# Kernel tuning notes

Hardware: AMD Instinct MI355X
Metric: run time of the kernel (lower is better)

The kernel has to match this reference:

```python
import jax, jax.numpy as jnp
import numpy as np

BN_EPS = 1e-5
POOL_EPS = 1e-6


def conv3x3(x, w, b):
    # x: (N,C,H,W), w: (O,C,3,3) -> (N,O,H,W), stride 1, SAME padding
    y = jax.lax.conv_general_dilated(x, w, window_strides=(1, 1), padding='SAME',
                                     dimension_numbers=('NCHW', 'OIHW', 'NCHW'))
    return y + b[None, :, None, None]


def deform_conv2d(x, off_w, off_b, mod_w, mod_b, w, b):
    # Modulated deformable conv (DCNv2), 3x3, stride 1, padding 1 (torchvision semantics).
    N, C, H, W = x.shape
    off = conv3x3(x, off_w, off_b).reshape(N, 9, 2, H, W)  # per-tap (dy, dx)
    mod = 2.0 * jax.nn.sigmoid(conv3x3(x, mod_w, mod_b))   # (N,9,H,W)
    dy = (jnp.arange(3, dtype=x.dtype) - 1.0).repeat(3)    # tap k = ky*3+kx
    dx = jnp.tile(jnp.arange(3, dtype=x.dtype) - 1.0, 3)
    py = off[:, :, 0] + dy[None, :, None, None] + jnp.arange(H, dtype=x.dtype)[None, None, :, None]
    px = off[:, :, 1] + dx[None, :, None, None] + jnp.arange(W, dtype=x.dtype)[None, None, None, :]
    y0f = jnp.floor(py); x0f = jnp.floor(px)
    wy = py - y0f; wx = px - x0f
    y0 = y0f.astype(jnp.int32); x0 = x0f.astype(jnp.int32)
    flat = x.reshape(N, C, H * W)

    def gather(yi, xi):
        # zero padding outside the image
        valid = ((yi >= 0) & (yi < H) & (xi >= 0) & (xi < W)).astype(x.dtype)
        idx = jnp.clip(yi, 0, H - 1) * W + jnp.clip(xi, 0, W - 1)      # (N,9,H,W)
        idx_b = jnp.broadcast_to(idx.reshape(N, 1, -1), (N, C, 9 * H * W))
        g = jnp.take_along_axis(flat, idx_b, axis=2).reshape(N, C, 9, H, W)
        return g * valid[:, None]

    s = (gather(y0, x0) * ((1 - wy) * (1 - wx))[:, None]
         + gather(y0, x0 + 1) * ((1 - wy) * wx)[:, None]
         + gather(y0 + 1, x0) * (wy * (1 - wx))[:, None]
         + gather(y0 + 1, x0 + 1) * (wy * wx)[:, None])       # (N,C,9,H,W)
    out = jnp.einsum('nckij,nkij,ock->noij', s, mod, w.reshape(w.shape[0], C, 9))
    return out + b[None, :, None, None]


def setup_inputs() -> dict:
    key = jax.random.key(0)
    ks = jax.random.split(key, 20)
    b, n_f, n_i, Hm, Wm = 2, 8, 10, 192, 192
    C_in, C_dcn, n_inc, n_pix = 256, 64, 128, 64
    h, w = 96, 96
    f32 = jnp.float32
    inp = {
        'x': jax.random.normal(ks[0], (b * n_f, C_in, h, w), f32),
        'masks': jax.random.uniform(ks[1], (b, n_f, n_i, Hm, Wm), f32),
        'conv1_w': jax.random.normal(ks[2], (C_dcn, C_in, 3, 3), f32) * 0.02,
        'conv1_b': jnp.zeros((C_dcn,), f32),
        'bn_gamma': jnp.ones((C_dcn,), f32),
        'bn_beta': jnp.zeros((C_dcn,), f32),
        'bn_mean': jax.random.normal(ks[3], (C_dcn,), f32) * 0.01,
        'bn_var': jnp.ones((C_dcn,), f32),
        'off_w': jax.random.normal(ks[4], (18, C_dcn, 3, 3), f32) * 0.01,
        'off_b': jnp.zeros((18,), f32),
        'mod_w': jax.random.normal(ks[5], (9, C_dcn, 3, 3), f32) * 0.01,
        'mod_b': jnp.zeros((9,), f32),
        'dcn_w': jax.random.normal(ks[6], (C_dcn, C_dcn, 3, 3), f32) * 0.05,
        'dcn_b': jnp.zeros((C_dcn,), f32),
        'smooth_w': jax.random.normal(ks[7], (C_dcn, C_dcn), f32) * 0.05,
        'smooth_b': jnp.zeros((C_dcn,), f32),
        'inc_w': jax.random.normal(ks[8], (n_inc, C_dcn), f32) * 0.05,
        'pix_w': jax.random.normal(ks[9], (n_pix, C_dcn), f32) * 0.05,
    }
    return inp


def reference(x, masks, conv1_w, conv1_b, bn_gamma, bn_beta, bn_mean, bn_var,
              off_w, off_b, mod_w, mod_b, dcn_w, dcn_b,
              smooth_w, smooth_b, inc_w, pix_w):
    # conv1: Conv3x3 + BatchNorm (eval stats) + ReLU
    y = conv3x3(x, conv1_w, conv1_b)
    y = (y - bn_mean[None, :, None, None]) * (bn_gamma[None, :, None, None]
        * jax.lax.rsqrt(bn_var + BN_EPS)[None, :, None, None]) + bn_beta[None, :, None, None]
    y = jax.nn.relu(y)
    # deformable conv
    y = deform_conv2d(y, off_w, off_b, mod_w, mod_b, dcn_w, dcn_b)

    b, n_f, n_i, Hm, Wm = masks.shape
    N, C, h, w = y.shape
    # resizeAnyShape -> bilinear, align_corners=False
    m = jax.image.resize(masks.reshape(b * n_f * n_i, Hm, Wm),
                         (b * n_f * n_i, h, w), method='bilinear', antialias=False)
    m = m.reshape(b, n_f, n_i, h * w)
    xf = y.reshape(b, n_f, C, h * w)
    # mask-weighted spatial average: avoid (b,n_f,n_i,C,h*w) intermediate
    num = jnp.einsum('bfcp,bfip->bfic', xf, m)            # (b,n_f,n_i,C)
    den = m.sum(axis=-1)[..., None]                        # (b,n_f,n_i,1)
    feat = num / (den + POOL_EPS)
    feat = jax.nn.relu(feat @ smooth_w.T + smooth_b)
    inc_kernels = feat @ inc_w.T
    pix_kernels = feat @ pix_w.T
    return (inc_kernels, pix_kernels)
```

## Files before the change

kernel.cpp:

```cpp
#include <hip/hip_runtime.h>
#include <hip/hip_bf16.h>

typedef __attribute__((ext_vector_type(8))) __bf16 bf16x8;
typedef __attribute__((ext_vector_type(4))) float f32x4;
typedef __attribute__((ext_vector_type(4))) unsigned int u32x4;
typedef __attribute__((ext_vector_type(4))) unsigned short u16x4;
typedef __attribute__((ext_vector_type(8))) unsigned short ushort8;
typedef __attribute__((ext_vector_type(4))) int i32x4;

#define MFMA16(a,b,c) __builtin_amdgcn_mfma_f32_16x16x32_bf16((a),(b),(c),0,0,0)

__device__ __forceinline__ float b2f(unsigned short u) {
  union { unsigned int i; float f; } v; v.i = ((unsigned int)u) << 16; return v.f;
}
__device__ __forceinline__ unsigned short f2b(float f) {
  union { float f; unsigned int u; } v; v.f = f;
  unsigned int u = v.u;
  unsigned int r = (u + 0x7fffu + ((u >> 16) & 1u)) >> 16;
  return (unsigned short)r;
}

#define NIMG 16
#define CIN  256
#define CD   64
#define HH   96
#define WW   96
#define HW   (HH*WW)

#define OFF_Y1   (0ll)
#define OFF_Y2   (18874368ll)
#define OFF_OFF  (37748736ll)
#define OFF_MOD  (48365568ll)
#define OFF_M    (53673984ll)
#define OFF_NP   OFF_OFF
#define OFF_DP   (OFF_OFF + 1310720ll)
#define OFF_SBN  (59908096ll)
#define OFF_TBN  (59908352ll)
#define OFF_W1   (59908608ll)
#define OFF_W2   (60203520ll)
#define OFF_W3   (60240384ll)
#define WS_NEEDED (60314112ll)

__global__ void k_prep(const float* __restrict__ conv1_w, const float* __restrict__ conv1_b,
                       const float* __restrict__ bn_gamma, const float* __restrict__ bn_beta,
                       const float* __restrict__ bn_mean, const float* __restrict__ bn_var,
                       const float* __restrict__ off_w, const float* __restrict__ mod_w,
                       const float* __restrict__ dcn_w,
                       unsigned short* __restrict__ w1, unsigned short* __restrict__ w2,
                       unsigned short* __restrict__ w3,
                       float* __restrict__ sbn, float* __restrict__ tbn)
{
  int e = blockIdx.x * 256 + threadIdx.x;
  if (e < 147456) {
    int j = e & 7, o = (e >> 3) & 63, cg = (e >> 9) & 31, t = e >> 14;
    w1[e] = f2b(conv1_w[(o * 256 + cg * 8 + j) * 9 + t]);
  } else if (e < 147456 + 18432) {
    int i = e - 147456;
    int j = i & 7, o = (i >> 3) & 31, cg = (i >> 8) & 7, t = i >> 11;
    int ch = cg * 8 + j;
    float v = 0.f;
    if (o < 18)      v = off_w[(o * 64 + ch) * 9 + t];
    else if (o < 27) v = mod_w[((o - 18) * 64 + ch) * 9 + t];
    w2[i] = f2b(v);
  } else if (e < 147456 + 18432 + 36864) {
    int i = e - 147456 - 18432;
    int j = i & 7, o = (i >> 3) & 63, cg = (i >> 9) & 7, t = i >> 12;
    w3[i] = f2b(dcn_w[(o * 64 + cg * 8 + j) * 9 + t]);
  } else {
    int i = e - (147456 + 18432 + 36864);
    if (i < 64) {
      sbn[i] = bn_gamma[i] * rsqrtf(bn_var[i] + 1e-5f);
    } else if (i < 128) {
      int q = i - 64;
      float s = bn_gamma[q] * rsqrtf(bn_var[q] + 1e-5f);
      tbn[q] = (conv1_b[q] - bn_mean[q]) * s + bn_beta[q];
    }
  }
}

__global__ __launch_bounds__(256)
void k_conv1(const float* __restrict__ x, const unsigned short* __restrict__ w1,
             const float* __restrict__ sbn, const float* __restrict__ tbn,
             unsigned short* __restrict__ y1)
{
  __shared__ __align__(16) unsigned short xs[4][98][48];
  __shared__ __align__(16) unsigned short As[9 * 4 * 64 * 8];

  const int tid = threadIdx.x;
  const int lane = tid & 63, wv = tid >> 6;
  const int l16 = lane & 15, lg = lane >> 4;
  const int wrow = wv & 1, wch = wv >> 1;
  const int h0 = blockIdx.x * 2;
  const int n = blockIdx.y;
  const float* xn = x + (size_t)n * CIN * HW;

  f32x4 acc[2][6];
  #pragma unroll
  for (int a = 0; a < 2; ++a)
    #pragma unroll
    for (int b = 0; b < 6; ++b) { f32x4 z = {0.f,0.f,0.f,0.f}; acc[a][b] = z; }

  for (int chunk = 0; chunk < 8; ++chunk) {
    const int c0 = chunk * 32;
    __syncthreads();
    #pragma unroll
    for (int it = 0; it < 12; ++it) {
      int idx = tid + it * 256;
      int c = idx & 31;
      int w4 = (idx >> 5) % 24;
      int r = idx / 768;
      int row = h0 - 1 + r;
      f32x4 v = {0.f,0.f,0.f,0.f};
      if (row >= 0 && row < HH)
        v = *reinterpret_cast<const f32x4*>(xn + (c0 + c) * HW + row * WW + w4 * 4);
      int wp = w4 * 4 + 1;
      xs[r][wp + 0][c] = f2b(v[0]);
      xs[r][wp + 1][c] = f2b(v[1]);
      xs[r][wp + 2][c] = f2b(v[2]);
      xs[r][wp + 3][c] = f2b(v[3]);
      if (w4 == 0)  xs[r][0][c]  = 0;
      if (w4 == 23) xs[r][97][c] = 0;
    }
    #pragma unroll
    for (int it = 0; it < 9; ++it) {
      int idx = tid + it * 256;
      int o = idx & 63, g = (idx >> 6) & 3, t = idx >> 8;
      *reinterpret_cast<u32x4*>(&As[((t * 4 + g) * 64 + o) * 8]) =
        *reinterpret_cast<const u32x4*>(&w1[((t * 32 + chunk * 4 + g) * 64 + o) * 8]);
    }
    __syncthreads();
    #pragma unroll
    for (int t = 0; t < 9; ++t) {
      const int ky = t / 3, kx = t % 3;
      bf16x8 a0 = *reinterpret_cast<const bf16x8*>(&As[((t*4 + lg)*64 + wch*32 + l16)*8]);
      bf16x8 a1 = *reinterpret_cast<const bf16x8*>(&As[((t*4 + lg)*64 + wch*32 + 16 + l16)*8]);
      const int r = wrow + ky;
      #pragma unroll
      for (int wt = 0; wt < 6; ++wt) {
        bf16x8 b = *reinterpret_cast<const bf16x8*>(&xs[r][wt*16 + l16 + kx][lg*8]);
        acc[0][wt] = MFMA16(a0, b, acc[0][wt]);
        acc[1][wt] = MFMA16(a1, b, acc[1][wt]);
      }
    }
  }
  __syncthreads();
  unsigned short* ys = &xs[0][0][0];
  #pragma unroll
  for (int ct = 0; ct < 2; ++ct) {
    #pragma unroll
    for (int j = 0; j < 4; ++j) {
      int o = wch * 32 + ct * 16 + lg * 4 + j;
      float s = sbn[o], tt = tbn[o];
      #pragma unroll
      for (int wt = 0; wt < 6; ++wt) {
        float v = acc[ct][wt][j] * s + tt;
        v = v > 0.f ? v : 0.f;
        ys[((wrow * 96 + wt * 16 + l16) * 72) + o] = f2b(v);
      }
    }
  }
  __syncthreads();
  #pragma unroll
  for (int it = 0; it < 6; ++it) {
    int idx = tid + it * 256;
    int cg = idx & 7, p = (idx >> 3) % 96, r = idx / 768;
    *reinterpret_cast<u32x4*>(&y1[(((size_t)(n * HH + h0 + r)) * WW + p) * 64 + cg * 8]) =
      *reinterpret_cast<const u32x4*>(&ys[(r * 96 + p) * 72 + cg * 8]);
  }
}

__global__ __launch_bounds__(256)
void k_conv2(const unsigned short* __restrict__ y1, const unsigned short* __restrict__ w2,
             const float* __restrict__ off_b, const float* __restrict__ mod_b,
             float* __restrict__ off_o, float* __restrict__ mod_o)
{
  __shared__ __align__(16) unsigned short xs[4][98][48];

  const int tid = threadIdx.x;
  const int lane = tid & 63, wv = tid >> 6;
  const int l16 = lane & 15, lg = lane >> 4;
  const int wrow = wv & 1, wct = wv >> 1;
  const int h0 = blockIdx.x * 2;
  const int n = blockIdx.y;
  const unsigned short* y1n = y1 + (size_t)n * HW * CD;

  bf16x8 aR[2][9];
  #pragma unroll
  for (int ch = 0; ch < 2; ++ch)
    #pragma unroll
    for (int t = 0; t < 9; ++t)
      aR[ch][t] = *reinterpret_cast<const bf16x8*>(
          &w2[((t * 8 + ch * 4 + lg) * 32 + wct * 16 + l16) * 8]);

  f32x4 acc[6];
  #pragma unroll
  for (int b = 0; b < 6; ++b) { f32x4 z = {0.f,0.f,0.f,0.f}; acc[b] = z; }

  #pragma unroll
  for (int chunk = 0; chunk < 2; ++chunk) {
    const int c0 = chunk * 32;
    __syncthreads();
    #pragma unroll
    for (int it = 0; it < 6; ++it) {
      int idx = tid + it * 256;
      int cg = idx & 3, w = (idx >> 2) % 96, r = idx / 384;
      int row = h0 - 1 + r;
      u32x4 v = {0u,0u,0u,0u};
      if (row >= 0 && row < HH)
        v = *reinterpret_cast<const u32x4*>(&y1n[((size_t)row * WW + w) * 64 + c0 + cg * 8]);
      *reinterpret_cast<u32x4*>(&xs[r][w + 1][cg * 8]) = v;
    }
    if (tid < 32) {
      int r = tid >> 3, side = (tid >> 2) & 1, cg = tid & 3;
      u32x4 z = {0u,0u,0u,0u};
      *reinterpret_cast<u32x4*>(&xs[r][side * 97][cg * 8]) = z;
    }
    __syncthreads();
    #pragma unroll
    for (int t = 0; t < 9; ++t) {
      const int ky = t / 3, kx = t % 3;
      const int r = wrow + ky;
      #pragma unroll
      for (int wt = 0; wt < 6; ++wt) {
        bf16x8 b = *reinterpret_cast<const bf16x8*>(&xs[r][wt*16 + l16 + kx][lg*8]);
        acc[wt] = MFMA16(aR[chunk][t], b, acc[wt]);
      }
    }
  }
  const int h = h0 + wrow;
  #pragma unroll
  for (int j = 0; j < 4; ++j) {
    int o = wct * 16 + lg * 4 + j;
    if (o < 18) {
      float bo = off_b[o];
      #pragma unroll
      for (int wt = 0; wt < 6; ++wt)
        off_o[((n * 18 + o) * HH + h) * WW + wt * 16 + l16] = acc[wt][j] + bo;
    } else if (o < 27) {
      int q = o - 18;
      float bo = mod_b[q];
      #pragma unroll
      for (int wt = 0; wt < 6; ++wt) {
        float v = acc[wt][j] + bo;
        mod_o[((n * 9 + q) * HH + h) * WW + wt * 16 + l16] = 2.f / (1.f + expf(-v));
      }
    }
  }
}

__global__ __launch_bounds__(256)
void k_dcn(const unsigned short* __restrict__ y1, const float* __restrict__ off_i,
           const float* __restrict__ mod_i, const unsigned short* __restrict__ w3,
           const float* __restrict__ dcn_b, unsigned short* __restrict__ y2)
{
  __shared__ __align__(16) f32x4 wgt[864];
  __shared__ __align__(16) i32x4 ofs[864];
  __shared__ __align__(16) unsigned short Bs[96][72];

  const int tid = threadIdx.x;
  const int lane = tid & 63, wv = tid >> 6;
  const int l16 = lane & 15, lg = lane >> 4;
  const int h = blockIdx.x, n = blockIdx.y;

  bf16x8 aW[9][2];
  #pragma unroll
  for (int t = 0; t < 9; ++t)
    #pragma unroll
    for (int kk = 0; kk < 2; ++kk)
      aW[t][kk] = *reinterpret_cast<const bf16x8*>(
          &w3[((t * 8 + kk * 4 + lg) * 64 + wv * 16 + l16) * 8]);

  #pragma unroll
  for (int it = 0; it < 4; ++it) {
    int e = tid + it * 256;
    if (e < 864) {
      int k = e / 96, p = e % 96;
      float dy = off_i[((n * 18 + 2 * k) * HH + h) * WW + p];
      float dx = off_i[((n * 18 + 2 * k + 1) * HH + h) * WW + p];
      float mw = mod_i[((n * 9 + k) * HH + h) * WW + p];
      float py = (float)(h + k / 3 - 1) + dy;
      float px = (float)(p + k % 3 - 1) + dx;
      float y0f = floorf(py), x0f = floorf(px);
      float wy = py - y0f, wx = px - x0f;
      int iy0 = (int)y0f, ix0 = (int)x0f;
      int iy1 = iy0 + 1, ix1 = ix0 + 1;
      float vy0 = (iy0 >= 0 && iy0 < HH) ? 1.f : 0.f;
      float vy1 = (iy1 >= 0 && iy1 < HH) ? 1.f : 0.f;
      float vx0 = (ix0 >= 0 && ix0 < WW) ? 1.f : 0.f;
      float vx1 = (ix1 >= 0 && ix1 < WW) ? 1.f : 0.f;
      f32x4 w4;
      w4[0] = (1.f - wy) * (1.f - wx) * mw * vy0 * vx0;
      w4[1] = (1.f - wy) * wx         * mw * vy0 * vx1;
      w4[2] = wy         * (1.f - wx) * mw * vy1 * vx0;
      w4[3] = wy         * wx         * mw * vy1 * vx1;
      wgt[e] = w4;
      int cy0 = iy0 < 0 ? 0 : (iy0 > 95 ? 95 : iy0);
      int cy1 = iy1 < 0 ? 0 : (iy1 > 95 ? 95 : iy1);
      int cx0 = ix0 < 0 ? 0 : (ix0 > 95 ? 95 : ix0);
      int cx1 = ix1 < 0 ? 0 : (ix1 > 95 ? 95 : ix1);
      i32x4 o4;
      o4[0] = (cy0 * WW + cx0) * 64; o4[1] = (cy0 * WW + cx1) * 64;
      o4[2] = (cy1 * WW + cx0) * 64; o4[3] = (cy1 * WW + cx1) * 64;
      ofs[e] = o4;
    }
  }
  __syncthreads();

  const unsigned short* y1n = y1 + (size_t)n * HW * CD;
  f32x4 acc[6];
  #pragma unroll
  for (int b = 0; b < 6; ++b) { f32x4 z = {0.f,0.f,0.f,0.f}; acc[b] = z; }

  #pragma unroll
  for (int t = 0; t < 9; ++t) {
    #pragma unroll
    for (int it = 0; it < 3; ++it) {
      int idx = tid + it * 256;
      int cg = idx & 7, p = idx >> 3;
      f32x4 w4 = wgt[t * 96 + p];
      i32x4 o4 = ofs[t * 96 + p];
      ushort8 g0 = *reinterpret_cast<const ushort8*>(&y1n[o4[0] + cg * 8]);
      ushort8 g1 = *reinterpret_cast<const ushort8*>(&y1n[o4[1] + cg * 8]);
      ushort8 g2 = *reinterpret_cast<const ushort8*>(&y1n[o4[2] + cg * 8]);
      ushort8 g3 = *reinterpret_cast<const ushort8*>(&y1n[o4[3] + cg * 8]);
      unsigned int wds[4];
      #pragma unroll
      for (int q = 0; q < 4; ++q) {
        float va = w4[0]*b2f(g0[2*q])   + w4[1]*b2f(g1[2*q])
                 + w4[2]*b2f(g2[2*q])   + w4[3]*b2f(g3[2*q]);
        float vb = w4[0]*b2f(g0[2*q+1]) + w4[1]*b2f(g1[2*q+1])
                 + w4[2]*b2f(g2[2*q+1]) + w4[3]*b2f(g3[2*q+1]);
        wds[q] = (unsigned int)f2b(va) | ((unsigned int)f2b(vb) << 16);
      }
      u32x4 pk = {wds[0], wds[1], wds[2], wds[3]};
      *reinterpret_cast<u32x4*>(&Bs[p][cg * 8]) = pk;
    }
    __syncthreads();
    #pragma unroll
    for (int kk = 0; kk < 2; ++kk) {
      #pragma unroll
      for (int wt = 0; wt < 6; ++wt) {
        bf16x8 b = *reinterpret_cast<const bf16x8*>(&Bs[wt * 16 + l16][kk * 32 + lg * 8]);
        acc[wt] = MFMA16(aW[t][kk], b, acc[wt]);
      }
    }
    __syncthreads();
  }

  unsigned short* Bs2 = reinterpret_cast<unsigned short*>(wgt);
  #pragma unroll
  for (int j = 0; j < 4; ++j) {
    int o = wv * 16 + lg * 4 + j;
    float bo = dcn_b[o];
    #pragma unroll
    for (int wt = 0; wt < 6; ++wt)
      Bs2[o * 104 + wt * 16 + l16] = f2b(acc[wt][j] + bo);
  }
  __syncthreads();
  #pragma unroll
  for (int it = 0; it < 3; ++it) {
    int idx = tid + it * 256;
    int seg = idx % 12, o = idx / 12;
    *reinterpret_cast<u32x4*>(&y2[(((size_t)n * CD + o) * HH + h) * WW + seg * 8]) =
      *reinterpret_cast<const u32x4*>(&Bs2[o * 104 + seg * 8]);
  }
}

__global__ void k_resize(const float* __restrict__ masks, float* __restrict__ m)
{
  int gid = blockIdx.x * 256 + threadIdx.x;
  if (gid >= 16 * 10 * HW) return;
  int pix = gid % HW;
  int r = gid / HW;
  int oh = pix / WW, ow = pix % WW;
  const float* s = masks + ((size_t)r * 192 + 2 * oh) * 192 + 2 * ow;
  m[gid] = 0.25f * (s[0] + s[1] + s[192] + s[193]);
}

__global__ __launch_bounds__(256)
void k_pool(const unsigned short* __restrict__ y2, const float* __restrict__ m,
            float* __restrict__ num_part, float* __restrict__ den_part)
{
  __shared__ float ms[10][288];
  __shared__ float red[4][10][64];
  __shared__ float den_red[10][16];
  const int tid = threadIdx.x;
  const int seg = blockIdx.x, bf = blockIdx.y;
  const int p0 = seg * 288;

  #pragma unroll
  for (int it = 0; it < 12; ++it) {
    int idx = tid + it * 256;
    if (idx < 2880) {
      int i = idx / 288, p = idx % 288;
      ms[i][p] = m[(bf * 10 + i) * HW + p0 + p];
    }
  }
  __syncthreads();

  const int c = tid & 63, grp = tid >> 6;
  float acc[10];
  #pragma unroll
  for (int i = 0; i < 10; ++i) acc[i] = 0.f;
  const unsigned short* yrow = y2 + (size_t)(bf * 64 + c) * HW + p0 + grp * 72;
  for (int qb = 0; qb < 18; ++qb) {
    u16x4 yv = *reinterpret_cast<const u16x4*>(yrow + qb * 4);
    float v0 = b2f(yv[0]), v1 = b2f(yv[1]), v2 = b2f(yv[2]), v3 = b2f(yv[3]);
    int pp = grp * 72 + qb * 4;
    #pragma unroll
    for (int i = 0; i < 10; ++i) {
      f32x4 mv = *reinterpret_cast<const f32x4*>(&ms[i][pp]);
      acc[i] += v0 * mv[0] + v1 * mv[1] + v2 * mv[2] + v3 * mv[3];
    }
  }
  #pragma unroll
  for (int i = 0; i < 10; ++i) red[grp][i][c] = acc[i];
  if (tid < 160) {
    int i = tid >> 4, s16 = tid & 15;
    float s = 0.f;
    for (int k2 = 0; k2 < 18; ++k2) s += ms[i][s16 + k2 * 16];
    den_red[i][s16] = s;
  }
  __syncthreads();
  #pragma unroll
  for (int it = 0; it < 3; ++it) {
    int e = tid + it * 256;
    if (e < 640) {
      int i = e >> 6, cc = e & 63;
      num_part[((bf * 32 + seg) * 10 + i) * 64 + cc] =
        red[0][i][cc] + red[1][i][cc] + red[2][i][cc] + red[3][i][cc];
    }
  }
  if (tid < 10) {
    float s = 0.f;
    for (int k2 = 0; k2 < 16; ++k2) s += den_red[tid][k2];
    den_part[(bf * 32 + seg) * 16 + tid] = s;
  }
}

__global__ void k_head(const float* __restrict__ num_part, const float* __restrict__ den_part,
                       const float* __restrict__ smooth_w, const float* __restrict__ smooth_b,
                       const float* __restrict__ inc_w, const float* __restrict__ pix_w,
                       float* __restrict__ out)
{
  __shared__ float pool_s[10][64];
  __shared__ float feat_s[10][64];
  const int tid = threadIdx.x;
  const int bf = blockIdx.x;
  #pragma unroll
  for (int it = 0; it < 3; ++it) {
    int e = tid + it * 256;
    if (e < 640) {
      int i = e >> 6, cc = e & 63;
      float nsum = 0.f, dsum = 0.f;
      for (int s = 0; s < 32; ++s) {
        nsum += num_part[((bf * 32 + s) * 10 + i) * 64 + cc];
        dsum += den_part[(bf * 32 + s) * 16 + i];
      }
      pool_s[i][cc] = nsum / (dsum + 1e-6f);
    }
  }
  __syncthreads();
  #pragma unroll
  for (int it = 0; it < 3; ++it) {
    int e = tid + it * 256;
    if (e < 640) {
      int i = e >> 6, cc = e & 63;
      float s = smooth_b[cc];
      for (int k = 0; k < 64; ++k) s += pool_s[i][k] * smooth_w[cc * 64 + k];
      feat_s[i][cc] = s > 0.f ? s : 0.f;
    }
  }
  __syncthreads();
  #pragma unroll
  for (int it = 0; it < 5; ++it) {
    int e = tid + it * 256;
    if (e < 1280) {
      int i = e >> 7, oc = e & 127;
      float s = 0.f;
      for (int k = 0; k < 64; ++k) s += feat_s[i][k] * inc_w[oc * 64 + k];
      out[(bf * 10 + i) * 128 + oc] = s;
    }
  }
  #pragma unroll
  for (int it = 0; it < 3; ++it) {
    int e = tid + it * 256;
    if (e < 640) {
      int i = e >> 6, oc = e & 63;
      float s = 0.f;
      for (int k = 0; k < 64; ++k) s += feat_s[i][k] * pix_w[oc * 64 + k];
      out[20480 + (bf * 10 + i) * 64 + oc] = s;
    }
  }
}

extern "C" void kernel_launch(void* const* d_in, const int* in_sizes, int n_in,
                              void* d_out, int out_size, void* d_ws, size_t ws_size,
                              hipStream_t stream)
{
  const float* x        = (const float*)d_in[0];
  const float* masks    = (const float*)d_in[1];
  const float* conv1_w  = (const float*)d_in[2];
  const float* conv1_b  = (const float*)d_in[3];
  const float* bn_gamma = (const float*)d_in[4];
  const float* bn_beta  = (const float*)d_in[5];
  const float* bn_mean  = (const float*)d_in[6];
  const float* bn_var   = (const float*)d_in[7];
  const float* off_w    = (const float*)d_in[8];
  const float* off_b    = (const float*)d_in[9];
  const float* mod_w    = (const float*)d_in[10];
  const float* mod_b    = (const float*)d_in[11];
  const float* dcn_w    = (const float*)d_in[12];
  const float* dcn_b    = (const float*)d_in[13];
  const float* smooth_w = (const float*)d_in[14];
  const float* smooth_b = (const float*)d_in[15];
  const float* inc_w    = (const float*)d_in[16];
  const float* pix_w    = (const float*)d_in[17];
  float* out = (float*)d_out;

  if (ws_size < (size_t)WS_NEEDED) return;
  char* ws = (char*)d_ws;
  unsigned short* y1  = (unsigned short*)(ws + OFF_Y1);
  unsigned short* y2  = (unsigned short*)(ws + OFF_Y2);
  float* off_t        = (float*)(ws + OFF_OFF);
  float* mod_t        = (float*)(ws + OFF_MOD);
  float* mbuf         = (float*)(ws + OFF_M);
  float* num_part     = (float*)(ws + OFF_NP);
  float* den_part     = (float*)(ws + OFF_DP);
  float* sbn          = (float*)(ws + OFF_SBN);
  float* tbn          = (float*)(ws + OFF_TBN);
  unsigned short* w1  = (unsigned short*)(ws + OFF_W1);
  unsigned short* w2  = (unsigned short*)(ws + OFF_W2);
  unsigned short* w3  = (unsigned short*)(ws + OFF_W3);

  k_prep<<<793, 256, 0, stream>>>(conv1_w, conv1_b, bn_gamma, bn_beta, bn_mean, bn_var,
                                  off_w, mod_w, dcn_w, w1, w2, w3, sbn, tbn);
  k_conv1<<<dim3(48, 16), 256, 0, stream>>>(x, w1, sbn, tbn, y1);
  k_conv2<<<dim3(48, 16), 256, 0, stream>>>(y1, w2, off_b, mod_b, off_t, mod_t);
  k_dcn<<<dim3(96, 16), 256, 0, stream>>>(y1, off_t, mod_t, w3, dcn_b, y2);
  k_resize<<<(16 * 10 * HW + 255) / 256, 256, 0, stream>>>(masks, mbuf);
  k_pool<<<dim3(32, 16), 256, 0, stream>>>(y2, mbuf, num_part, den_part);
  k_head<<<16, 256, 0, stream>>>(num_part, den_part, smooth_w, smooth_b, inc_w, pix_w, out);
}
```

Before: 509.9 us.

## Pre-transpose input to channels-last bf16, pack DCN metadata, switch y2 to NHWC

```diff
diff --git a/kernel.cpp b/kernel.cpp
--- a/kernel.cpp
+++ b/kernel.cpp
@@ -4,9 +4,9 @@
 typedef __attribute__((ext_vector_type(8))) __bf16 bf16x8;
 typedef __attribute__((ext_vector_type(4))) float f32x4;
 typedef __attribute__((ext_vector_type(4))) unsigned int u32x4;
+typedef __attribute__((ext_vector_type(2))) unsigned int u32x2;
 typedef __attribute__((ext_vector_type(4))) unsigned short u16x4;
 typedef __attribute__((ext_vector_type(8))) unsigned short ushort8;
-typedef __attribute__((ext_vector_type(4))) int i32x4;
 
 #define MFMA16(a,b,c) __builtin_amdgcn_mfma_f32_16x16x32_bf16((a),(b),(c),0,0,0)
 
@@ -18,6 +18,12 @@
   unsigned int u = v.u;
   unsigned int r = (u + 0x7fffu + ((u >> 16) & 1u)) >> 16;
   return (unsigned short)r;
+}
+__device__ __forceinline__ unsigned short f2h(float f) {
+  _Float16 x = (_Float16)f; unsigned short r; __builtin_memcpy(&r, &x, 2); return r;
+}
+__device__ __forceinline__ float h2f(unsigned short h) {
+  _Float16 x; __builtin_memcpy(&x, &h, 2); return (float)x;
 }
 
 #define NIMG 16
@@ -79,20 +85,48 @@
 }
 
 __global__ __launch_bounds__(256)
-void k_conv1(const float* __restrict__ x, const unsigned short* __restrict__ w1,
-             const float* __restrict__ sbn, const float* __restrict__ tbn,
-             unsigned short* __restrict__ y1)
-{
-  __shared__ __align__(16) unsigned short xs[4][98][48];
-  __shared__ __align__(16) unsigned short As[9 * 4 * 64 * 8];
+void k_tr(const float* __restrict__ x, unsigned short* __restrict__ xT, int n_base)
+{
+  __shared__ __align__(16) unsigned short ls[64][68];
+  const int tid = threadIdx.x;
+  const int p0 = blockIdx.x * 64, c0 = blockIdx.y * 64, nl = blockIdx.z;
+  const float* xn = x + (size_t)(n_base + nl) * CIN * HW;
+
+  const int p4 = tid & 15, cb = tid >> 4;
+  #pragma unroll
+  for (int it = 0; it < 4; ++it) {
+    int c = cb + it * 16;
+    f32x4 v = *reinterpret_cast<const f32x4*>(xn + (size_t)(c0 + c) * HW + p0 + p4 * 4);
+    #pragma unroll
+    for (int q = 0; q < 4; ++q) ls[p4 * 4 + q][c] = f2b(v[q]);
+  }
+  __syncthreads();
+  const int cg = tid & 7, pb = tid >> 3;
+  #pragma unroll
+  for (int it = 0; it < 2; ++it) {
+    int p = pb + it * 32;
+    u32x2 lo = *reinterpret_cast<const u32x2*>(&ls[p][cg * 8]);
+    u32x2 hi = *reinterpret_cast<const u32x2*>(&ls[p][cg * 8 + 4]);
+    u32x4 v = {lo[0], lo[1], hi[0], hi[1]};
+    *reinterpret_cast<u32x4*>(&xT[((size_t)nl * HW + p0 + p) * CIN + c0 + cg * 8]) = v;
+  }
+}
+
+__global__ __launch_bounds__(256)
+void k_conv1t(const unsigned short* __restrict__ xT, const unsigned short* __restrict__ w1,
+              const float* __restrict__ sbn, const float* __restrict__ tbn,
+              unsigned short* __restrict__ y1, int n_base)
+{
+  __shared__ __align__(16) unsigned short xs[4][98][40];
 
   const int tid = threadIdx.x;
   const int lane = tid & 63, wv = tid >> 6;
   const int l16 = lane & 15, lg = lane >> 4;
   const int wrow = wv & 1, wch = wv >> 1;
   const int h0 = blockIdx.x * 2;
-  const int n = blockIdx.y;
-  const float* xn = x + (size_t)n * CIN * HW;
+  const int nl = blockIdx.y;
+  const int n = n_base + nl;
+  const unsigned short* xn = xT + (size_t)nl * HW * CIN;
 
   f32x4 acc[2][6];
   #pragma unroll
@@ -104,36 +138,28 @@
     const int c0 = chunk * 32;
     __syncthreads();
     #pragma unroll
-    for (int it = 0; it < 12; ++it) {
+    for (int it = 0; it < 6; ++it) {
       int idx = tid + it * 256;
-      int c = idx & 31;
-      int w4 = (idx >> 5) % 24;
-      int r = idx / 768;
+      int cg = idx & 3, w = (idx >> 2) % 96, r = idx / 384;
       int row = h0 - 1 + r;
-      f32x4 v = {0.f,0.f,0.f,0.f};
+      u32x4 v = {0u,0u,0u,0u};
       if (row >= 0 && row < HH)
-        v = *reinterpret_cast<const f32x4*>(xn + (c0 + c) * HW + row * WW + w4 * 4);
-      int wp = w4 * 4 + 1;
-      xs[r][wp + 0][c] = f2b(v[0]);
-      xs[r][wp + 1][c] = f2b(v[1]);
-      xs[r][wp + 2][c] = f2b(v[2]);
-      xs[r][wp + 3][c] = f2b(v[3]);
-      if (w4 == 0)  xs[r][0][c]  = 0;
-      if (w4 == 23) xs[r][97][c] = 0;
-    }
-    #pragma unroll
-    for (int it = 0; it < 9; ++it) {
-      int idx = tid + it * 256;
-      int o = idx & 63, g = (idx >> 6) & 3, t = idx >> 8;
-      *reinterpret_cast<u32x4*>(&As[((t * 4 + g) * 64 + o) * 8]) =
-        *reinterpret_cast<const u32x4*>(&w1[((t * 32 + chunk * 4 + g) * 64 + o) * 8]);
+        v = *reinterpret_cast<const u32x4*>(&xn[((size_t)row * WW + w) * CIN + c0 + cg * 8]);
+      *reinterpret_cast<u32x4*>(&xs[r][w + 1][cg * 8]) = v;
+    }
+    if (tid < 32) {
+      int r = tid >> 3, side = (tid >> 2) & 1, cg = tid & 3;
+      u32x4 z = {0u,0u,0u,0u};
+      *reinterpret_cast<u32x4*>(&xs[r][side * 97][cg * 8]) = z;
     }
     __syncthreads();
     #pragma unroll
     for (int t = 0; t < 9; ++t) {
       const int ky = t / 3, kx = t % 3;
-      bf16x8 a0 = *reinterpret_cast<const bf16x8*>(&As[((t*4 + lg)*64 + wch*32 + l16)*8]);
-      bf16x8 a1 = *reinterpret_cast<const bf16x8*>(&As[((t*4 + lg)*64 + wch*32 + 16 + l16)*8]);
+      bf16x8 a0 = *reinterpret_cast<const bf16x8*>(
+          &w1[((t * 32 + chunk * 4 + lg) * 64 + wch * 32 + l16) * 8]);
+      bf16x8 a1 = *reinterpret_cast<const bf16x8*>(
+          &w1[((t * 32 + chunk * 4 + lg) * 64 + wch * 32 + 16 + l16) * 8]);
       const int r = wrow + ky;
       #pragma unroll
       for (int wt = 0; wt < 6; ++wt) {
@@ -147,16 +173,19 @@
   unsigned short* ys = &xs[0][0][0];
   #pragma unroll
   for (int ct = 0; ct < 2; ++ct) {
-    #pragma unroll
-    for (int j = 0; j < 4; ++j) {
-      int o = wch * 32 + ct * 16 + lg * 4 + j;
-      float s = sbn[o], tt = tbn[o];
-      #pragma unroll
-      for (int wt = 0; wt < 6; ++wt) {
-        float v = acc[ct][wt][j] * s + tt;
-        v = v > 0.f ? v : 0.f;
-        ys[((wrow * 96 + wt * 16 + l16) * 72) + o] = f2b(v);
-      }
+    int o4 = wch * 32 + ct * 16 + lg * 4;
+    f32x4 s4 = *reinterpret_cast<const f32x4*>(&sbn[o4]);
+    f32x4 t4 = *reinterpret_cast<const f32x4*>(&tbn[o4]);
+    #pragma unroll
+    for (int wt = 0; wt < 6; ++wt) {
+      int p = wrow * 96 + wt * 16 + l16;
+      float v0 = acc[ct][wt][0] * s4[0] + t4[0]; v0 = v0 > 0.f ? v0 : 0.f;
+      float v1 = acc[ct][wt][1] * s4[1] + t4[1]; v1 = v1 > 0.f ? v1 : 0.f;
+      float v2 = acc[ct][wt][2] * s4[2] + t4[2]; v2 = v2 > 0.f ? v2 : 0.f;
+      float v3 = acc[ct][wt][3] * s4[3] + t4[3]; v3 = v3 > 0.f ? v3 : 0.f;
+      u32x2 d = {(unsigned)f2b(v0) | ((unsigned)f2b(v1) << 16),
+                 (unsigned)f2b(v2) | ((unsigned)f2b(v3) << 16)};
+      *reinterpret_cast<u32x2*>(&ys[p * 72 + o4]) = d;
     }
   }
   __syncthreads();
@@ -164,7 +193,7 @@
   for (int it = 0; it < 6; ++it) {
     int idx = tid + it * 256;
     int cg = idx & 7, p = (idx >> 3) % 96, r = idx / 768;
-    *reinterpret_cast<u32x4*>(&y1[(((size_t)(n * HH + h0 + r)) * WW + p) * 64 + cg * 8]) =
+    *reinterpret_cast<u32x4*>(&y1[(((size_t)n * HH + h0 + r) * WW + p) * CD + cg * 8]) =
       *reinterpret_cast<const u32x4*>(&ys[(r * 96 + p) * 72 + cg * 8]);
   }
 }
@@ -174,7 +203,7 @@
              const float* __restrict__ off_b, const float* __restrict__ mod_b,
              float* __restrict__ off_o, float* __restrict__ mod_o)
 {
-  __shared__ __align__(16) unsigned short xs[4][98][48];
+  __shared__ __align__(16) unsigned short xs[4][98][40];
 
   const int tid = threadIdx.x;
   const int lane = tid & 63, wv = tid >> 6;
@@ -184,14 +213,6 @@
   const int n = blockIdx.y;
   const unsigned short* y1n = y1 + (size_t)n * HW * CD;
 
-  bf16x8 aR[2][9];
-  #pragma unroll
-  for (int ch = 0; ch < 2; ++ch)
-    #pragma unroll
-    for (int t = 0; t < 9; ++t)
-      aR[ch][t] = *reinterpret_cast<const bf16x8*>(
-          &w2[((t * 8 + ch * 4 + lg) * 32 + wct * 16 + l16) * 8]);
-
   f32x4 acc[6];
   #pragma unroll
   for (int b = 0; b < 6; ++b) { f32x4 z = {0.f,0.f,0.f,0.f}; acc[b] = z; }
@@ -199,6 +220,11 @@
   #pragma unroll
   for (int chunk = 0; chunk < 2; ++chunk) {
     const int c0 = chunk * 32;
+    bf16x8 aR[9];
+    #pragma unroll
+    for (int t = 0; t < 9; ++t)
+      aR[t] = *reinterpret_cast<const bf16x8*>(
+          &w2[((t * 8 + chunk * 4 + lg) * 32 + wct * 16 + l16) * 8]);
     __syncthreads();
     #pragma unroll
     for (int it = 0; it < 6; ++it) {
@@ -207,7 +233,7 @@
       int row = h0 - 1 + r;
       u32x4 v = {0u,0u,0u,0u};
       if (row >= 0 && row < HH)
-        v = *reinterpret_cast<const u32x4*>(&y1n[((size_t)row * WW + w) * 64 + c0 + cg * 8]);
+        v = *reinterpret_cast<const u32x4*>(&y1n[((size_t)row * WW + w) * CD + c0 + cg * 8]);
       *reinterpret_cast<u32x4*>(&xs[r][w + 1][cg * 8]) = v;
     }
     if (tid < 32) {
@@ -223,7 +249,7 @@
       #pragma unroll
       for (int wt = 0; wt < 6; ++wt) {
         bf16x8 b = *reinterpret_cast<const bf16x8*>(&xs[r][wt*16 + l16 + kx][lg*8]);
-        acc[wt] = MFMA16(aR[chunk][t], b, acc[wt]);
+        acc[wt] = MFMA16(aR[t], b, acc[wt]);
       }
     }
   }
@@ -250,25 +276,16 @@
 
 __global__ __launch_bounds__(256)
 void k_dcn(const unsigned short* __restrict__ y1, const float* __restrict__ off_i,
-           const float* __restrict__ mod_i, const unsigned short* __restrict__ w3,
+           const float* __restrict__ mod_i, const unsigned short* __restrict__ w3g,
            const float* __restrict__ dcn_b, unsigned short* __restrict__ y2)
 {
-  __shared__ __align__(16) f32x4 wgt[864];
-  __shared__ __align__(16) i32x4 ofs[864];
+  __shared__ __align__(16) unsigned short meta[864][8];
   __shared__ __align__(16) unsigned short Bs[96][72];
 
   const int tid = threadIdx.x;
   const int lane = tid & 63, wv = tid >> 6;
   const int l16 = lane & 15, lg = lane >> 4;
   const int h = blockIdx.x, n = blockIdx.y;
-
-  bf16x8 aW[9][2];
-  #pragma unroll
-  for (int t = 0; t < 9; ++t)
-    #pragma unroll
-    for (int kk = 0; kk < 2; ++kk)
-      aW[t][kk] = *reinterpret_cast<const bf16x8*>(
-          &w3[((t * 8 + kk * 4 + lg) * 64 + wv * 16 + l16) * 8]);
 
   #pragma unroll
   for (int it = 0; it < 4; ++it) {
@@ -288,20 +305,19 @@
       float vy1 = (iy1 >= 0 && iy1 < HH) ? 1.f : 0.f;
       float vx0 = (ix0 >= 0 && ix0 < WW) ? 1.f : 0.f;
       float vx1 = (ix1 >= 0 && ix1 < WW) ? 1.f : 0.f;
-      f32x4 w4;
-      w4[0] = (1.f - wy) * (1.f - wx) * mw * vy0 * vx0;
-      w4[1] = (1.f - wy) * wx         * mw * vy0 * vx1;
-      w4[2] = wy         * (1.f - wx) * mw * vy1 * vx0;
-      w4[3] = wy         * wx         * mw * vy1 * vx1;
-      wgt[e] = w4;
+      unsigned short m0 = f2h((1.f - wy) * (1.f - wx) * mw * vy0 * vx0);
+      unsigned short m1 = f2h((1.f - wy) * wx         * mw * vy0 * vx1);
+      unsigned short m2 = f2h(wy         * (1.f - wx) * mw * vy1 * vx0);
+      unsigned short m3 = f2h(wy         * wx         * mw * vy1 * vx1);
       int cy0 = iy0 < 0 ? 0 : (iy0 > 95 ? 95 : iy0);
       int cy1 = iy1 < 0 ? 0 : (iy1 > 95 ? 95 : iy1);
       int cx0 = ix0 < 0 ? 0 : (ix0 > 95 ? 95 : ix0);
       int cx1 = ix1 < 0 ? 0 : (ix1 > 95 ? 95 : ix1);
-      i32x4 o4;
-      o4[0] = (cy0 * WW + cx0) * 64; o4[1] = (cy0 * WW + cx1) * 64;
-      o4[2] = (cy1 * WW + cx0) * 64; o4[3] = (cy1 * WW + cx1) * 64;
-      ofs[e] = o4;
+      u32x4 pk = {(unsigned)m0 | ((unsigned)m1 << 16),
+                  (unsigned)m2 | ((unsigned)m3 << 16),
+                  (unsigned)(cy0 * WW + cx0) | ((unsigned)(cy0 * WW + cx1) << 16),
+                  (unsigned)(cy1 * WW + cx0) | ((unsigned)(cy1 * WW + cx1) << 16)};
+      *reinterpret_cast<u32x4*>(&meta[e][0]) = pk;
     }
   }
   __syncthreads();
@@ -313,23 +329,34 @@
 
   #pragma unroll
   for (int t = 0; t < 9; ++t) {
+    bf16x8 a0 = *reinterpret_cast<const bf16x8*>(
+        &w3g[((t * 8 + lg) * 64 + wv * 16 + l16) * 8]);
+    bf16x8 a1 = *reinterpret_cast<const bf16x8*>(
+        &w3g[((t * 8 + 4 + lg) * 64 + wv * 16 + l16) * 8]);
     #pragma unroll
     for (int it = 0; it < 3; ++it) {
       int idx = tid + it * 256;
       int cg = idx & 7, p = idx >> 3;
-      f32x4 w4 = wgt[t * 96 + p];
-      i32x4 o4 = ofs[t * 96 + p];
-      ushort8 g0 = *reinterpret_cast<const ushort8*>(&y1n[o4[0] + cg * 8]);
-      ushort8 g1 = *reinterpret_cast<const ushort8*>(&y1n[o4[1] + cg * 8]);
-      ushort8 g2 = *reinterpret_cast<const ushort8*>(&y1n[o4[2] + cg * 8]);
-      ushort8 g3 = *reinterpret_cast<const ushort8*>(&y1n[o4[3] + cg * 8]);
+      u32x4 mk = *reinterpret_cast<const u32x4*>(&meta[t * 96 + p][0]);
+      float hw0 = h2f((unsigned short)(mk[0] & 0xffffu));
+      float hw1 = h2f((unsigned short)(mk[0] >> 16));
+      float hw2 = h2f((unsigned short)(mk[1] & 0xffffu));
+      float hw3 = h2f((unsigned short)(mk[1] >> 16));
+      int o0 = (int)(mk[2] & 0xffffu) << 6;
+      int o1 = (int)(mk[2] >> 16) << 6;
+      int o2 = (int)(mk[3] & 0xffffu) << 6;
+      int o3 = (int)(mk[3] >> 16) << 6;
+      ushort8 g0 = *reinterpret_cast<const ushort8*>(&y1n[o0 + cg * 8]);
+      ushort8 g1 = *reinterpret_cast<const ushort8*>(&y1n[o1 + cg * 8]);
+      ushort8 g2 = *reinterpret_cast<const ushort8*>(&y1n[o2 + cg * 8]);
+      ushort8 g3 = *reinterpret_cast<const ushort8*>(&y1n[o3 + cg * 8]);
       unsigned int wds[4];
       #pragma unroll
       for (int q = 0; q < 4; ++q) {
-        float va = w4[0]*b2f(g0[2*q])   + w4[1]*b2f(g1[2*q])
-                 + w4[2]*b2f(g2[2*q])   + w4[3]*b2f(g3[2*q]);
-        float vb = w4[0]*b2f(g0[2*q+1]) + w4[1]*b2f(g1[2*q+1])
-                 + w4[2]*b2f(g2[2*q+1]) + w4[3]*b2f(g3[2*q+1]);
+        float va = hw0*b2f(g0[2*q])   + hw1*b2f(g1[2*q])
+                 + hw2*b2f(g2[2*q])   + hw3*b2f(g3[2*q]);
+        float vb = hw0*b2f(g0[2*q+1]) + hw1*b2f(g1[2*q+1])
+                 + hw2*b2f(g2[2*q+1]) + hw3*b2f(g3[2*q+1]);
         wds[q] = (unsigned int)f2b(va) | ((unsigned int)f2b(vb) << 16);
       }
       u32x4 pk = {wds[0], wds[1], wds[2], wds[3]};
@@ -337,32 +364,34 @@
     }
     __syncthreads();
     #pragma unroll
-    for (int kk = 0; kk < 2; ++kk) {
-      #pragma unroll
-      for (int wt = 0; wt < 6; ++wt) {
-        bf16x8 b = *reinterpret_cast<const bf16x8*>(&Bs[wt * 16 + l16][kk * 32 + lg * 8]);
-        acc[wt] = MFMA16(aW[t][kk], b, acc[wt]);
-      }
+    for (int wt = 0; wt < 6; ++wt) {
+      bf16x8 b0 = *reinterpret_cast<const bf16x8*>(&Bs[wt * 16 + l16][lg * 8]);
+      bf16x8 b1 = *reinterpret_cast<const bf16x8*>(&Bs[wt * 16 + l16][32 + lg * 8]);
+      acc[wt] = MFMA16(a0, b0, acc[wt]);
+      acc[wt] = MFMA16(a1, b1, acc[wt]);
     }
     __syncthreads();
   }
 
-  unsigned short* Bs2 = reinterpret_cast<unsigned short*>(wgt);
-  #pragma unroll
-  for (int j = 0; j < 4; ++j) {
-    int o = wv * 16 + lg * 4 + j;
-    float bo = dcn_b[o];
-    #pragma unroll
-    for (int wt = 0; wt < 6; ++wt)
-      Bs2[o * 104 + wt * 16 + l16] = f2b(acc[wt][j] + bo);
+  unsigned short* Bs2 = &Bs[0][0];
+  {
+    int o4 = wv * 16 + lg * 4;
+    f32x4 b4 = *reinterpret_cast<const f32x4*>(&dcn_b[o4]);
+    #pragma unroll
+    for (int wt = 0; wt < 6; ++wt) {
+      int p = wt * 16 + l16;
+      u32x2 d = {(unsigned)f2b(acc[wt][0] + b4[0]) | ((unsigned)f2b(acc[wt][1] + b4[1]) << 16),
+                 (unsigned)f2b(acc[wt][2] + b4[2]) | ((unsigned)f2b(acc[wt][3] + b4[3]) << 16)};
+      *reinterpret_cast<u32x2*>(&Bs2[p * 72 + o4]) = d;
+    }
   }
   __syncthreads();
   #pragma unroll
   for (int it = 0; it < 3; ++it) {
     int idx = tid + it * 256;
-    int seg = idx % 12, o = idx / 12;
-    *reinterpret_cast<u32x4*>(&y2[(((size_t)n * CD + o) * HH + h) * WW + seg * 8]) =
-      *reinterpret_cast<const u32x4*>(&Bs2[o * 104 + seg * 8]);
+    int cg = idx & 7, p = idx >> 3;
+    *reinterpret_cast<u32x4*>(&y2[(((size_t)n * HH + h) * WW + p) * CD + cg * 8]) =
+      *reinterpret_cast<const u32x4*>(&Bs2[p * 72 + cg * 8]);
   }
 }
 
@@ -402,16 +431,11 @@
   float acc[10];
   #pragma unroll
   for (int i = 0; i < 10; ++i) acc[i] = 0.f;
-  const unsigned short* yrow = y2 + (size_t)(bf * 64 + c) * HW + p0 + grp * 72;
-  for (int qb = 0; qb < 18; ++qb) {
-    u16x4 yv = *reinterpret_cast<const u16x4*>(yrow + qb * 4);
-    float v0 = b2f(yv[0]), v1 = b2f(yv[1]), v2 = b2f(yv[2]), v3 = b2f(yv[3]);
-    int pp = grp * 72 + qb * 4;
-    #pragma unroll
-    for (int i = 0; i < 10; ++i) {
-      f32x4 mv = *reinterpret_cast<const f32x4*>(&ms[i][pp]);
-      acc[i] += v0 * mv[0] + v1 * mv[1] + v2 * mv[2] + v3 * mv[3];
-    }
+  const unsigned short* yb = y2 + ((size_t)bf * HW + p0 + grp * 72) * CD + c;
+  for (int p = 0; p < 72; ++p) {
+    float v = b2f(yb[p * CD]);
+    #pragma unroll
+    for (int i = 0; i < 10; ++i) acc[i] += v * ms[i][grp * 72 + p];
   }
   #pragma unroll
   for (int i = 0; i < 10; ++i) red[grp][i][c] = acc[i];
@@ -522,6 +546,7 @@
   char* ws = (char*)d_ws;
   unsigned short* y1  = (unsigned short*)(ws + OFF_Y1);
   unsigned short* y2  = (unsigned short*)(ws + OFF_Y2);
+  unsigned short* xT  = (unsigned short*)(ws + OFF_Y2);
   float* off_t        = (float*)(ws + OFF_OFF);
   float* mod_t        = (float*)(ws + OFF_MOD);
   float* mbuf         = (float*)(ws + OFF_M);
@@ -535,7 +560,11 @@
 
   k_prep<<<793, 256, 0, stream>>>(conv1_w, conv1_b, bn_gamma, bn_beta, bn_mean, bn_var,
                                   off_w, mod_w, dcn_w, w1, w2, w3, sbn, tbn);
-  k_conv1<<<dim3(48, 16), 256, 0, stream>>>(x, w1, sbn, tbn, y1);
+  for (int pass = 0; pass < 2; ++pass) {
+    int n_base = pass * 8;
+    k_tr<<<dim3(144, 4, 8), 256, 0, stream>>>(x, xT, n_base);
+    k_conv1t<<<dim3(48, 8), 256, 0, stream>>>(xT, w1, sbn, tbn, y1, n_base);
+  }
   k_conv2<<<dim3(48, 16), 256, 0, stream>>>(y1, w2, off_b, mod_b, off_t, mod_t);
   k_dcn<<<dim3(96, 16), 256, 0, stream>>>(y1, off_t, mod_t, w3, dcn_b, y2);
   k_resize<<<(16 * 10 * HW + 255) / 256, 256, 0, stream>>>(masks, mbuf);
```

After: 486.3 us. 1.05x faster.
